# Kernel tuning notes

Hardware: AMD Instinct MI355X
Metric: run time of the kernel (lower is better)

The kernel has to match this reference:

```python
import jax, jax.numpy as jnp
import numpy as np

N = 500
PX = 1e-6
WAVELENGTH = 0.561e-6
FOCAL = 6e-3
LASER_FWHC = 2e-4
N_REFR = 1.33
K = 2.0 * N_REFR * np.pi / WAVELENGTH          # wavenumber
MAX_INTENSITY = 50000.0
UNIF_BG = 100.0
NOISE_MEAN = 3e8
NOISE_STD = 2e8
MAX_VAL = 4e9
PATCH = 31                                      # PSF patch is 31x31


def _constants():
    x = np.arange(-N // 2, N // 2)
    X, Y = np.meshgrid(x, x)
    X = X * PX; Y = Y * PX
    C1 = (np.pi / (WAVELENGTH * FOCAL) * (X ** 2 + Y ** 2)) % (2 * np.pi)
    B1 = np.exp(-1j * C1).astype(np.complex64)
    mask_real = np.exp(-(X ** 2 + Y ** 2) / (2 * LASER_FWHC ** 2)).astype(np.float32)
    xx = np.arange(-N + 1, N + 1)
    XX, YY = np.meshgrid(xx, xx)
    XX = XX * PX; YY = YY * PX
    Q1 = np.exp(1j * (np.pi * N_REFR / (WAVELENGTH * FOCAL)) * (XX ** 2 + YY ** 2)).astype(np.complex64)
    Fs = 1.0 / PX
    F = np.arange(-Fs / 2, Fs / 2, Fs / N)
    alpha = N_REFR * WAVELENGTH * F
    A, B = np.meshgrid(alpha, alpha)
    gamma = np.sqrt(1.0 - A ** 2 - B ** 2).astype(np.float32)
    return B1, mask_real, Q1, gamma


def setup_inputs() -> dict:
    key = jax.random.key(0)
    k1, k2, k3, k4, k5, k6, k7 = jax.random.split(key, 7)
    B1, mask_real, Q1, gamma = _constants()
    Bsz, E = 2, 64
    mask_param = jax.random.normal(k1, (N, N), jnp.float32)
    xy = jax.random.randint(k2, (Bsz, E, 2), 15, 185)       # patch centers inside 200x200 canvas
    z = jax.random.randint(k3, (Bsz, E, 1), 0, 31)          # defocus index, 31 PSF planes
    xyz = jnp.concatenate([xy, z], axis=-1).astype(jnp.int32)
    nphotons = jax.random.uniform(k4, (Bsz, E), jnp.float32)  # unused by forward (as in source)
    psf_imgs = jax.random.uniform(k5, (31, PATCH, PATCH), jnp.float32)  # stand-in for beads_img_defocus tiffs
    noise_gauss = jax.random.normal(k6, (Bsz, 1, 200, 200), jnp.float32)
    noise_poiss = jax.random.normal(k7, (Bsz, 1, 200, 200), jnp.float32)
    return {
        "mask_param": mask_param, "xyz": xyz, "nphotons": nphotons,
        "B1": jnp.asarray(B1), "Q1": jnp.asarray(Q1),
        "mask_real": jnp.asarray(mask_real), "gamma_cust": jnp.asarray(gamma),
        "psf_imgs": psf_imgs, "noise_gauss": noise_gauss, "noise_poiss": noise_poiss,
    }


def _forward(mask_param, xyz, nphotons, B1, Q1, mask_real, gamma_cust,
             psf_imgs, noise_gauss, noise_poiss):
    Bsz, E, _ = xyz.shape
    # phase mask applied to laser beam profile
    M = mask_real * jnp.exp(1j * mask_param)                 # (N,N) complex
    field = B1 * M
    E1 = jnp.pad(field, ((250, 250), (250, 250)))            # (2N,2N)
    E2 = jnp.fft.ifftshift(jnp.fft.ifft2(jnp.fft.fft2(E1) * jnp.fft.fft2(Q1)))
    out = E2[N // 2:3 * N // 2, N // 2:3 * N // 2]           # (N,N) complex
    Fout = jnp.fft.fftshift(jnp.fft.fft2(out))               # shared spectrum

    xs = (xyz[..., 0] - 100).reshape(-1).astype(jnp.float32)  # per-emitter defocus distance
    zs = xyz[..., 2].reshape(-1)

    def emitter_intensity(xf, zi):
        phase = jnp.exp(1j * (K * 1e-6) * gamma_cust * xf)
        U = jnp.fft.ifft2(jnp.fft.ifftshift(Fout * phase))
        I = jnp.real(U * jnp.conj(U))                        # (N,N)
        col = jax.lax.dynamic_slice_in_dim(I, 249 + zi, 1, axis=1)
        return jnp.sum(col)

    intens = jax.vmap(emitter_intensity)(xs, zs).reshape(Bsz, E)

    # per-emitter 31x31 PSF patch scaled by intensity, scatter-added onto 200x200 canvas
    patches = psf_imgs[jnp.abs(xyz[..., 2])] * intens[..., None, None]  # (B,E,31,31)
    d = jnp.arange(-15, 16)
    rows = xyz[..., 0][..., None] + d                        # (B,E,31)
    cols = xyz[..., 1][..., None] + d
    bidx = jnp.arange(Bsz)[:, None, None, None]
    canvas = jnp.zeros((Bsz, 200, 200), jnp.float32)
    canvas = canvas.at[bidx, rows[:, :, :, None], cols[:, :, None, :]].add(patches)
    imgs3D = canvas[:, None] / MAX_INTENSITY                 # (B,1,200,200)

    # NoiseLayer: uniform bg + gaussian-approximated poisson noise
    inp = imgs3D + UNIF_BG
    inp = inp + 1e5 + (NOISE_STD * noise_gauss + NOISE_MEAN)
    inp = jnp.where(inp <= 0, 0.0, inp)
    noisy = inp + 100.0 * jnp.sqrt(inp) * noise_poiss

    # Normalize01
    noisy = jnp.where(noisy <= 10.0, 1.0, noisy)
    noisy = jnp.minimum(noisy, MAX_VAL)
    return noisy / MAX_VAL


def reference(mask_param, xyz, nphotons, B1, Q1, mask_real, gamma_cust,
              psf_imgs, noise_gauss, noise_poiss):
    return _forward(mask_param, xyz, nphotons, B1, Q1, mask_real, gamma_cust,
                    psf_imgs, noise_gauss, noise_poiss)
```

## Files before the change

kernel.cpp:

```cpp
#include <hip/hip_runtime.h>
#include <math.h>


__device__ __forceinline__ float2 cmulf(float2 a, float2 b) {
  return make_float2(a.x * b.x - a.y * b.y, a.x * b.y + a.y * b.x);
}

template <int N>
__device__ __forceinline__ void build_tw_lds(float2* tw, int tid, int nthr) {
  const float inv = 1.0f / (float)N;
  for (int k = tid; k < N; k += nthr) {
    float fr = (float)k * inv;
    tw[k] = make_float2(__builtin_amdgcn_cosf(fr),
                        -__builtin_amdgcn_sinf(fr));
  }
}

template <int NFFT, int INV>
__device__ __forceinline__ float2* fft_core_g(float2* X, float2* Y,
                                              const float2* tw, int tid,
                                              int tstride, int twstride) {
  int Ns = 1;
  const int NF = (NFFT == 1000) ? 6 : 5;
  const int N2 = (NFFT == 1000) ? 3 : 2;
  const float W5r[5] = {1.f, 0.30901699f, -0.80901699f, -0.80901699f,
                        0.30901699f};
  const float W5i[5] = {0.f, INV ? 0.95105652f : -0.95105652f,
                        INV ? 0.58778525f : -0.58778525f,
                        INV ? -0.58778525f : 0.58778525f,
                        INV ? -0.95105652f : 0.95105652f};
  for (int p = 0; p < NF; ++p) {
    const int R = (p < N2) ? 2 : 5;
    const int NR = NFFT / R;
    const int stepk = NFFT / (Ns * R);
    for (int j = tid; j < NR; j += tstride) {
      const int jm = j % Ns;
      const int jd = j / Ns;
      const int idxD = jd * (Ns * R) + jm;
      if (R == 2) {
        float2 v0 = X[j];
        float2 w = tw[jm * stepk * twstride];
        if (INV) w.y = -w.y;
        float2 v1 = cmulf(X[j + NR], w);
        Y[idxD] = make_float2(v0.x + v1.x, v0.y + v1.y);
        Y[idxD + Ns] = make_float2(v0.x - v1.x, v0.y - v1.y);
      } else {
        float2 v[5];
        v[0] = X[j];
#pragma unroll
        for (int s = 1; s < 5; ++s) {
          float2 w = tw[jm * s * stepk * twstride];
          if (INV) w.y = -w.y;
          v[s] = cmulf(X[j + s * NR], w);
        }
#pragma unroll
        for (int t5 = 0; t5 < 5; ++t5) {
          float ax = v[0].x, ay = v[0].y;
#pragma unroll
          for (int s = 1; s < 5; ++s) {
            const int m = (s * t5) % 5;
            ax += v[s].x * W5r[m] - v[s].y * W5i[m];
            ay += v[s].x * W5i[m] + v[s].y * W5r[m];
          }
          Y[idxD + t5 * Ns] = make_float2(ax, ay);
        }
      }
    }
    __syncthreads();
    float2* t = X;
    X = Y;
    Y = t;
    Ns *= R;
  }
  return X;
}

__global__ __launch_bounds__(256) void e1_fft_kernel(
    const float* __restrict__ mask_param, const float* __restrict__ mask_real,
    float2* __restrict__ A, float2* __restrict__ qv) {
  __shared__ float2 bufA[1000];
  __shared__ float2 bufB[1000];
  __shared__ float2 twl[1000];
  const int b = blockIdx.x;
  const int tid = threadIdx.x;
  if (b >= 500 && b < 1000) {
    int k = b - 500;
    int rr = (k < 250) ? k : (k + 500);
    float2* dst = A + (size_t)rr * 1000;
    for (int i = tid; i < 1000; i += 256) dst[i] = make_float2(0.f, 0.f);
    return;
  }
  build_tw_lds<1000>(twl, tid, 256);
  if (b == 1000) {
    for (int i = tid; i < 1000; i += 256) {
      double xv = (double)(i - 499) * 1e-6;
      const double s2rev = 1.33 / (2.0 * 5.61e-7 * 0.006);
      double t = s2rev * xv * xv;
      float fr = (float)(t - floor(t));
      bufA[i] =
          make_float2(__builtin_amdgcn_cosf(fr), __builtin_amdgcn_sinf(fr));
    }
    __syncthreads();
    float2* X = fft_core_g<1000, 0>(bufA, bufB, twl, tid, 256, 1);
    for (int i = tid; i < 1000; i += 256) qv[i] = X[i];
    return;
  }
  const int rm = b;
  for (int i = tid; i < 1000; i += 256) {
    float2 val = make_float2(0.f, 0.f);
    if (i >= 250 && i < 750) {
      int cm = i - 250;
      int p = rm * 500 + cm;
      double xv = (double)(cm - 250) * 1e-6;
      double yv = (double)(rm - 250) * 1e-6;
      const double s1rev = 1.0 / (2.0 * 5.61e-7 * 0.006);
      double t = s1rev * (xv * xv + yv * yv);
      float fr = (float)(t - floor(t));
      float cb = __builtin_amdgcn_cosf(fr);
      float sb = __builtin_amdgcn_sinf(fr);
      float th = mask_param[p];
      float s, co;
      __sincosf(th, &s, &co);
      float m = mask_real[p];
      val = make_float2(m * (cb * co + sb * s), m * (cb * s - sb * co));
    }
    bufA[i] = val;
  }
  __syncthreads();
  float2* X = fft_core_g<1000, 0>(bufA, bufB, twl, tid, 256, 1);
  float2* dst = A + (size_t)(rm + 250) * 1000;
  for (int i = tid; i < 1000; i += 256) dst[i] = X[i];
}

__global__ __launch_bounds__(128) void colmul1000_kernel(
    float2* A, const float2* __restrict__ qv) {
  __shared__ float2 cA[2000];
  __shared__ float2 cB[2000];
  __shared__ float2 twl[1000];
  __shared__ float2 qh[1000];
  const int tid = threadIdx.x;
  const int cl = tid >> 6, lane = tid & 63;
  const int c0 = blockIdx.x * 2;
  build_tw_lds<1000>(twl, tid, 128);
  for (int i = tid; i < 1000; i += 128) qh[i] = qv[i];
  for (int idx = tid; idx < 2000; idx += 128) {
    int r = idx >> 1, cc = idx & 1;
    cA[cc * 1000 + r] = A[(size_t)r * 1000 + c0 + cc];
  }
  __syncthreads();
  float2* X = fft_core_g<1000, 0>(cA + cl * 1000, cB + cl * 1000, twl, lane,
                                  64, 1);
  float2 qc = qh[c0 + cl];
  qc.x *= 1e-6f;
  qc.y *= 1e-6f;
  for (int j = lane; j < 1000; j += 64) X[j] = cmulf(X[j], cmulf(qc, qh[j]));
  __syncthreads();
  float2* Y = (X == cA + cl * 1000) ? (cB + cl * 1000) : (cA + cl * 1000);
  fft_core_g<1000, 1>(X, Y, twl, lane, 64, 1);
  for (int idx = tid; idx < 2000; idx += 128) {
    int r = idx >> 1, cc = idx & 1;
    A[(size_t)r * 1000 + c0 + cc] = cA[cc * 1000 + r];
  }
}

__global__ __launch_bounds__(256) void ifft_crop_fft500_kernel(
    const float2* __restrict__ A, float2* __restrict__ C5) {
  __shared__ float2 bufA[1000];
  __shared__ float2 bufB[1000];
  __shared__ float2 twl[1000];
  const int r = blockIdx.x;
  const int rr = (750 + r) % 1000;
  const int tid = threadIdx.x;
  build_tw_lds<1000>(twl, tid, 256);
  const float2* src = A + (size_t)rr * 1000;
  for (int i = tid; i < 1000; i += 256) bufA[i] = src[i];
  __syncthreads();
  float2* X = fft_core_g<1000, 1>(bufA, bufB, twl, tid, 256, 1);
  float2* Y = (X == bufA) ? bufB : bufA;
  for (int c = tid; c < 500; c += 256) {
    int cc = (c < 250) ? (750 + c) : (c - 250);
    Y[c] = X[cc];
  }
  __syncthreads();
  float2* Z = fft_core_g<500, 0>(Y, X, twl, tid, 256, 2);
  float2* dst = C5 + (size_t)r * 500;
  for (int i = tid; i < 500; i += 256) dst[i] = Z[i];
}

__global__ __launch_bounds__(256) void col500_fout_kernel(
    const float2* __restrict__ C5, float2* __restrict__ Fout,
    float* __restrict__ canvas) {
  __shared__ float2 cA[2000];
  __shared__ float2 cB[2000];
  __shared__ float2 twl[500];
  const int bid = blockIdx.x;
  const int tid = threadIdx.x;
  if (bid >= 125) {
    int i = (bid - 125) * 256 + tid;
    if (i < 80000) canvas[i] = 0.f;
    return;
  }
  const int cl = tid >> 6, lane = tid & 63;
  const int c0 = bid * 4;
  build_tw_lds<500>(twl, tid, 256);
  for (int idx = tid; idx < 2000; idx += 256) {
    int r = idx >> 2, cc = idx & 3;
    cA[cc * 500 + r] = C5[(size_t)r * 500 + c0 + cc];
  }
  __syncthreads();
  fft_core_g<500, 0>(cA + cl * 500, cB + cl * 500, twl, lane, 64,
                     1);
  for (int idx = tid; idx < 2000; idx += 256) {
    int u = idx >> 2, cc = idx & 3;
    int v = (c0 + cc + 250) % 500;
    Fout[(size_t)u * 500 + v] = cB[cc * 500 + (u + 250) % 500];
  }
}

__global__ void fill_out_kernel(float* __restrict__ out, int n) {
  int i = blockIdx.x * blockDim.x + threadIdx.x;
  if (i < n) out[i] = 0.f;
}

__global__ __launch_bounds__(64) void emitter_partial_kernel(
    const float2* __restrict__ Fout, const float* __restrict__ gamma,
    const int* __restrict__ xyz, float* __restrict__ partial) {
  const int u = blockIdx.x;
  const int eg = blockIdx.y;
  const int lane = threadIdx.x;
  const float krev = 2.37076648841354f;
  const float2* Frow = Fout + u * 500;
  const float* grow = gamma + u * 500;
  float fx[8], fy[8], gg[8];
#pragma unroll
  for (int k = 0; k < 8; ++k) {
    int v = lane + 64 * k;
    if (v < 500) {
      float2 F = Frow[v];
      fx[k] = F.x;
      fy[k] = F.y;
      gg[k] = grow[v];
    } else {
      fx[k] = 0.f;
      fy[k] = 0.f;
      gg[k] = 0.f;
    }
  }
#pragma unroll 1
  for (int i = 0; i < 16; ++i) {
    const int e = eg * 16 + i;
    const float xf = (float)(xyz[e * 3 + 0] - 100);
    const int zc = 249 + xyz[e * 3 + 2];
    const float gx = krev * xf;
    int m = (zc * lane) % 500;
    const int step = (zc * 64) % 500;
    float ax = 0.f, ay = 0.f;
#pragma unroll
    for (int k = 0; k < 8; ++k) {
      float rev = fmaf(gx, gg[k], (float)m * 0.002f);
      float r = rev - floorf(rev);
      float s = __builtin_amdgcn_sinf(r);
      float co = __builtin_amdgcn_cosf(r);
      ax += fx[k] * co - fy[k] * s;
      ay += fx[k] * s + fy[k] * co;
      m += step;
      if (m >= 500) m -= 500;
    }
#pragma unroll
    for (int off = 1; off < 64; off <<= 1) {
      ax += __shfl_xor(ax, off, 64);
      ay += __shfl_xor(ay, off, 64);
    }
    if (lane == 0) partial[e * 500 + u] = (ax * ax + ay * ay) * 8.0e-9f;
  }
}

__global__ __launch_bounds__(256) void emitter_reduce_scatter_kernel(
    const float* __restrict__ partial, const float* __restrict__ psf,
    const int* __restrict__ xyz, float* __restrict__ canvas) {
  const int e = blockIdx.x;
  const int tid = threadIdx.x;
  __shared__ float red[4];
  float s = 0.f;
  for (int k = tid; k < 500; k += 256) s += partial[e * 500 + k];
#pragma unroll
  for (int off = 1; off < 64; off <<= 1) s += __shfl_xor(s, off, 64);
  if ((tid & 63) == 0) red[tid >> 6] = s;
  __syncthreads();
  const float inten = red[0] + red[1] + red[2] + red[3];
  const int x = xyz[e * 3 + 0];
  const int y = xyz[e * 3 + 1];
  const int z = xyz[e * 3 + 2];
  const int zz = (z < 0) ? -z : z;
  const int b = e >> 6;
  for (int t = tid; t < 961; t += 256) {
    int i = t / 31, j = t % 31;
    atomicAdd(&canvas[b * 40000 + (x - 15 + i) * 200 + (y - 15 + j)],
              psf[zz * 961 + t] * inten);
  }
}

__global__ void final_kernel(const float* __restrict__ canvas,
                             const float* __restrict__ ng,
                             const float* __restrict__ npz,
                             float* __restrict__ out) {
  int idx = blockIdx.x * blockDim.x + threadIdx.x;
  if (idx >= 80000) return;
  float inp = canvas[idx] / 50000.0f + 100.0f;
  inp = inp + 100000.0f + (2.0e8f * ng[idx] + 3.0e8f);
  if (inp <= 0.0f) inp = 0.0f;
  float noisy = inp + 100.0f * sqrtf(inp) * npz[idx];
  noisy = (noisy <= 10.0f) ? 1.0f : noisy;
  noisy = fminf(noisy, 4.0e9f);
  out[idx] = noisy / 4.0e9f;
}

extern "C" void kernel_launch(void* const* d_in, const int* in_sizes, int n_in,
                              void* d_out, int out_size, void* d_ws,
                              size_t ws_size, hipStream_t stream) {
  const float* mask_param = (const float*)d_in[0];
  const int* xyz = (const int*)d_in[1];
  const float* mask_real = (const float*)d_in[5];
  const float* gamma = (const float*)d_in[6];
  const float* psf = (const float*)d_in[7];
  const float* ng = (const float*)d_in[8];
  const float* npz = (const float*)d_in[9];
  float* out = (float*)d_out;

  char* p = (char*)d_ws;
  auto carve = [&](size_t bytes) -> char* {
    char* r = p;
    p += (bytes + 255) & ~(size_t)255;
    return r;
  };
  float2* A = (float2*)carve(1000 * 1000 * sizeof(float2));
  float2* C5 = (float2*)carve(500 * 500 * sizeof(float2));
  float2* Fn = (float2*)carve(500 * 500 * sizeof(float2));
  float* partial = (float*)carve(128 * 500 * sizeof(float));
  float2* qv = (float2*)carve(1000 * sizeof(float2));
  float* canvas = (float*)carve(80000 * sizeof(float));
  size_t need = (size_t)(p - (char*)d_ws);
  if (ws_size < need) {
    fill_out_kernel<<<(out_size + 255) / 256, 256, 0, stream>>>(out, out_size);
    return;
  }

  e1_fft_kernel<<<1001, 256, 0, stream>>>(mask_param, mask_real, A, qv);
  colmul1000_kernel<<<500, 128, 0, stream>>>(A, qv);
  ifft_crop_fft500_kernel<<<500, 256, 0, stream>>>(A, C5);
  col500_fout_kernel<<<438, 256, 0, stream>>>(C5, Fn, canvas);

  dim3 eg(500, 8);
  emitter_partial_kernel<<<eg, 64, 0, stream>>>(Fn, gamma, xyz, partial);
  emitter_reduce_scatter_kernel<<<128, 256, 0, stream>>>(partial, psf, xyz,
                                                         canvas);
  final_kernel<<<313, 256, 0, stream>>>(canvas, ng, npz, out);
}
```

Baseline: 175.1 us.

## Skip known-zero and unused rows in column FFT pass, one column per block

The first kernel no longer writes zeros into the padded rows of the 1000x1000 buffer. The column kernel instead treats rows outside 250..749 as zero when loading, and writes back only the rows that the later crop kernel reads. The column kernel now processes one column per 256-thread block instead of two columns per 128-thread block, with an interleaved column-to-block mapping. This roughly halves global traffic in that stage and removes the zero-fill. Each block now does strided single-column accesses, and the column kernel launches twice as many blocks.

```diff
diff --git a/kernel.cpp b/kernel.cpp
--- a/kernel.cpp
+++ b/kernel.cpp
@@ -83,15 +83,8 @@
   __shared__ float2 twl[1000];
   const int b = blockIdx.x;
   const int tid = threadIdx.x;
-  if (b >= 500 && b < 1000) {
-    int k = b - 500;
-    int rr = (k < 250) ? k : (k + 500);
-    float2* dst = A + (size_t)rr * 1000;
-    for (int i = tid; i < 1000; i += 256) dst[i] = make_float2(0.f, 0.f);
-    return;
-  }
   build_tw_lds<1000>(twl, tid, 256);
-  if (b == 1000) {
+  if (b == 500) {
     for (int i = tid; i < 1000; i += 256) {
       double xv = (double)(i - 499) * 1e-6;
       const double s2rev = 1.33 / (2.0 * 5.61e-7 * 0.006);
@@ -132,34 +125,31 @@
   for (int i = tid; i < 1000; i += 256) dst[i] = X[i];
 }
 
-__global__ __launch_bounds__(128) void colmul1000_kernel(
+__global__ __launch_bounds__(256) void colmul1000_kernel(
     float2* A, const float2* __restrict__ qv) {
-  __shared__ float2 cA[2000];
-  __shared__ float2 cB[2000];
+  __shared__ float2 bufA[1000];
+  __shared__ float2 bufB[1000];
   __shared__ float2 twl[1000];
-  __shared__ float2 qh[1000];
-  const int tid = threadIdx.x;
-  const int cl = tid >> 6, lane = tid & 63;
-  const int c0 = blockIdx.x * 2;
-  build_tw_lds<1000>(twl, tid, 128);
-  for (int i = tid; i < 1000; i += 128) qh[i] = qv[i];
-  for (int idx = tid; idx < 2000; idx += 128) {
-    int r = idx >> 1, cc = idx & 1;
-    cA[cc * 1000 + r] = A[(size_t)r * 1000 + c0 + cc];
-  }
-  __syncthreads();
-  float2* X = fft_core_g<1000, 0>(cA + cl * 1000, cB + cl * 1000, twl, lane,
-                                  64, 1);
-  float2 qc = qh[c0 + cl];
+  const int tid = threadIdx.x;
+  const int b = blockIdx.x;
+  const int c = (b & 7) * 125 + (b >> 3);
+  build_tw_lds<1000>(twl, tid, 256);
+  for (int r = tid; r < 1000; r += 256) {
+    float2 v = make_float2(0.f, 0.f);
+    if (r >= 250 && r < 750) v = A[(size_t)r * 1000 + c];
+    bufA[r] = v;
+  }
+  __syncthreads();
+  float2* X = fft_core_g<1000, 0>(bufA, bufB, twl, tid, 256, 1);
+  float2 qc = qv[c];
   qc.x *= 1e-6f;
   qc.y *= 1e-6f;
-  for (int j = lane; j < 1000; j += 64) X[j] = cmulf(X[j], cmulf(qc, qh[j]));
-  __syncthreads();
-  float2* Y = (X == cA + cl * 1000) ? (cB + cl * 1000) : (cA + cl * 1000);
-  fft_core_g<1000, 1>(X, Y, twl, lane, 64, 1);
-  for (int idx = tid; idx < 2000; idx += 128) {
-    int r = idx >> 1, cc = idx & 1;
-    A[(size_t)r * 1000 + c0 + cc] = cA[cc * 1000 + r];
+  for (int j = tid; j < 1000; j += 256) X[j] = cmulf(X[j], cmulf(qc, qv[j]));
+  __syncthreads();
+  float2* Y = (X == bufA) ? bufB : bufA;
+  float2* Z = fft_core_g<1000, 1>(X, Y, twl, tid, 256, 1);
+  for (int r = tid; r < 1000; r += 256) {
+    if (r < 250 || r >= 750) A[(size_t)r * 1000 + c] = Z[r];
   }
 }
 
@@ -345,8 +335,8 @@
     return;
   }
 
-  e1_fft_kernel<<<1001, 256, 0, stream>>>(mask_param, mask_real, A, qv);
-  colmul1000_kernel<<<500, 128, 0, stream>>>(A, qv);
+  e1_fft_kernel<<<501, 256, 0, stream>>>(mask_param, mask_real, A, qv);
+  colmul1000_kernel<<<1000, 256, 0, stream>>>(A, qv);
   ifft_crop_fft500_kernel<<<500, 256, 0, stream>>>(A, C5);
   col500_fout_kernel<<<438, 256, 0, stream>>>(C5, Fn, canvas);
 
```

Result: faster. 152.3 us (-13.0%).
